# Kernel optimization log

Hardware: AMD Instinct MI355X
Metric: run time of the kernel (lower is better)

Reference implementation:

```python
import jax, jax.numpy as jnp
import numpy as np

B, S, D = 2, 2048, 2048
H, G = 32, 8            # n_head, n_kv_groups
DH = D // H             # 64
HG = H // G             # heads per group = 4


def setup_inputs() -> dict:
    key = jax.random.key(0)
    ks = jax.random.split(key, 7)
    kv_dim = G * DH
    return {
        "q": jax.random.normal(ks[0], (B, S, D), jnp.float32),
        "k": jax.random.normal(ks[1], (B, S, D), jnp.float32),
        "v": jax.random.normal(ks[2], (B, S, D), jnp.float32),
        "mask": jnp.tril(jnp.ones((S, S), jnp.bool_)),  # causal
        "w_q": jax.random.normal(ks[3], (D, D), jnp.float32) * 0.02,
        "w_k": jax.random.normal(ks[4], (kv_dim, D), jnp.float32) * 0.02,
        "w_v": jax.random.normal(ks[5], (kv_dim, D), jnp.float32) * 0.02,
        "w_out": jax.random.normal(ks[6], (D, D), jnp.float32) * 0.02,
    }


def reference(q, k, v, mask, w_q, w_k, w_v, w_out):
    scale = 1.0 / np.sqrt(DH).astype(np.float32)
    # projections (F.linear: x @ W.T)
    qp = (q @ w_q.T).reshape(B, S, G, HG, DH)   # [b s g h d]
    kp = (k @ w_k.T).reshape(B, S, G, DH)       # [b t g d]
    vp = (v @ w_v.T).reshape(B, S, G, DH)
    # grouped attention scores [b g h s t]
    scores = jnp.einsum('bsghd,btgd->bghst', qp, kp) * scale
    scores = jnp.where(mask[None, None, None], scores, jnp.float32(-jnp.inf))
    attn = jax.nn.softmax(scores, axis=-1)
    out = jnp.einsum('bghst,btgd->bsghd', attn, vp).reshape(B, S, D)
    return out @ w_out.T
```

## Files before the change

kernel.cpp:

```cpp
#include <hip/hip_runtime.h>
#include <hip/hip_bf16.h>
#include <stdint.h>

#define B_SZ 2
#define S_LEN 2048
#define D_MODEL 2048
#define NH 32
#define NG 8
#define HGRP 4
#define DHEAD 64
#define KV_DIM 512
#define M_TOK 4096
#define KVB 64
#define QBLK 256
#define N_ITEMS2 768

typedef __attribute__((ext_vector_type(8))) short bf16x8;
typedef __attribute__((ext_vector_type(4))) float f32x4;
typedef __attribute__((ext_vector_type(16))) float f32x16;

__device__ inline unsigned short f2bf(float x) {
    uint32_t u = __builtin_bit_cast(uint32_t, x);
    uint32_t r = (u + 0x7fffu + ((u >> 16) & 1u)) >> 16;
    return (unsigned short)r;
}

__device__ inline uint32_t cvtpk(float lo, float hi) {
    uint32_t r;
    asm("v_cvt_pk_bf16_f32 %0, %1, %2" : "=v"(r) : "v"(lo), "v"(hi));
    return r;
}

__device__ inline void plswap(uint32_t& a, uint32_t& b) {
    asm volatile("v_permlane32_swap_b32 %0, %1" : "+v"(a), "+v"(b));
}

__device__ inline float bf2f(unsigned short u) {
    uint32_t x = ((uint32_t)u) << 16;
    return __builtin_bit_cast(float, x);
}

__device__ inline void async_copy16(const void* g, void* l) {
    __builtin_amdgcn_global_load_lds(
        (const __attribute__((address_space(1))) void*)g,
        (__attribute__((address_space(3))) void*)l,
        16, 0, 0);
}

__device__ inline void gbar() {
    asm volatile("" ::: "memory");
    __builtin_amdgcn_s_barrier();
    asm volatile("" ::: "memory");
}
__device__ inline void lgkm0() {
    asm volatile("s_waitcnt lgkmcnt(0)" ::: "memory");
    __builtin_amdgcn_sched_barrier(0);
}

__global__ __launch_bounds__(256) void cvt_all(const float* __restrict__ q,
                                               const float* __restrict__ k,
                                               const float* __restrict__ v,
                                               const float* __restrict__ wq,
                                               const float* __restrict__ wk,
                                               const float* __restrict__ wv,
                                               const float* __restrict__ wo,
                                               unsigned short* __restrict__ qb,
                                               unsigned short* __restrict__ kb,
                                               unsigned short* __restrict__ vb,
                                               unsigned short* __restrict__ wqb,
                                               unsigned short* __restrict__ wkvb,
                                               unsigned short* __restrict__ wob,
                                               unsigned int* __restrict__ cnt) {
    const int i = blockIdx.x * 256 + threadIdx.x;
    if (i == 0) *cnt = 0u;
    const float* src; unsigned short* dst; int j;
    if (i < 1048576)      { src = q;  dst = qb;  j = i; }
    else if (i < 2097152) { src = k;  dst = kb;  j = i - 1048576; }
    else if (i < 3145728) { src = v;  dst = vb;  j = i - 2097152; }
    else if (i < 3670016) { src = wq; dst = wqb; j = i - 3145728; }
    else if (i < 3801088) { src = wk; dst = wkvb; j = i - 3670016; }
    else if (i < 3932160) { src = wv; dst = wkvb + (size_t)KV_DIM * D_MODEL; j = i - 3801088; }
    else                  { src = wo; dst = wob; j = i - 3932160; }
    const float4* p = reinterpret_cast<const float4*>(src) + (size_t)j * 2;
    float4 a = p[0], b = p[1];
    union { unsigned short u[8]; uint4 v4; } r;
    r.u[0] = f2bf(a.x); r.u[1] = f2bf(a.y); r.u[2] = f2bf(a.z); r.u[3] = f2bf(a.w);
    r.u[4] = f2bf(b.x); r.u[5] = f2bf(b.y); r.u[6] = f2bf(b.z); r.u[7] = f2bf(b.w);
    reinterpret_cast<uint4*>(dst)[j] = r.v4;
}

#define SCALE_Q 0.1803368867f
#define GK 2048

__global__ __launch_bounds__(512, 2) void gemm8p(const unsigned short* __restrict__ Aq,
                                                 const unsigned short* __restrict__ Ak,
                                                 const unsigned short* __restrict__ Av,
                                                 const unsigned short* __restrict__ Bq,
                                                 const unsigned short* __restrict__ Bkv,
                                                 unsigned short* __restrict__ out_q,
                                                 unsigned short* __restrict__ out_k,
                                                 unsigned short* __restrict__ out_v) {
    __shared__ __align__(16) char lds[131072];

    const int tid = threadIdx.x;
    const int lane = tid & 63;
    const int w = tid >> 6;
    const int wm = w >> 2, wn = w & 3;
    const int l15 = lane & 15, l4 = lane >> 4;

    int bid = blockIdx.x;
    bid = (bid & 7) * 24 + (bid >> 3);
    const int mb = bid & 15, nb = bid >> 4;
    const int m0 = mb * 256;

    const unsigned short* Ap;
    const unsigned short* Bp;
    int mode = 0, n0q = 0;
    if (nb < 8) {
        Ap = Aq; Bp = Bq + (size_t)(nb * 256) * GK; mode = 0; n0q = nb * 256;
    } else if (nb < 10) {
        Ap = Ak; Bp = Bkv + (size_t)((nb - 8) * 256) * GK; mode = 1; n0q = (nb - 8) * 256;
    } else {
        Ap = Av; Bp = Bkv + (size_t)((nb - 10) * 256 + 512) * GK; mode = 2; n0q = (nb - 10) * 256;
    }

    const int srow = tid >> 3;
    const int gcol = (((tid & 7) * 16) ^ ((srow & 7) << 4)) >> 1;
    char* const myl = lds + tid * 16;

    auto stageA = [&](int tile, int half) {
        char* dst = myl + (tile & 1) * 32768 + half * 16384;
        const unsigned short* src = Ap + (size_t)(m0 + half * 128 + srow) * GK + tile * 64 + gcol;
        async_copy16(src, dst);
        async_copy16(src + (size_t)64 * GK, dst + 8192);
    };
    auto stageB = [&](int tile, int half) {
        char* dst = myl + 65536 + (tile & 1) * 32768 + half * 16384;
        const unsigned short* src = Bp + (size_t)(half * 128 + srow) * GK + tile * 64 + gcol;
        async_copy16(src, dst);
        async_copy16(src + (size_t)64 * GK, dst + 8192);
    };

    bf16x8 af[4][2], bf[4][2];
    auto loadA = [&](int buf, int mhalf) {
        const char* base = lds + buf * 32768;
#pragma unroll
        for (int mi = 0; mi < 4; ++mi) {
            const int r = wm * 128 + mhalf * 64 + mi * 16 + l15;
#pragma unroll
            for (int ks = 0; ks < 2; ++ks)
                af[mi][ks] = *reinterpret_cast<const bf16x8*>(
                    base + r * 128 + ((ks * 64 + l4 * 16) ^ ((r & 7) << 4)));
        }
    };
    auto loadB = [&](int buf, int nhalf) {
        const char* base = lds + 65536 + buf * 32768;
#pragma unroll
        for (int ni2 = 0; ni2 < 2; ++ni2) {
            const int ni = nhalf * 2 + ni2;
            const int r = wn * 64 + ni * 16 + l15;
#pragma unroll
            for (int ks = 0; ks < 2; ++ks)
                bf[ni][ks] = *reinterpret_cast<const bf16x8*>(
                    base + r * 128 + ((ks * 64 + l4 * 16) ^ ((r & 7) << 4)));
        }
    };

    f32x4 acc[8][4] = {};
    auto mfma16 = [&](int mq, int nq) {
        __builtin_amdgcn_s_setprio(1);
#pragma unroll
        for (int mi = 0; mi < 4; ++mi)
#pragma unroll
            for (int ni2 = 0; ni2 < 2; ++ni2)
#pragma unroll
                for (int ks = 0; ks < 2; ++ks)
                    acc[mq * 4 + mi][nq * 2 + ni2] = __builtin_amdgcn_mfma_f32_16x16x32_bf16(
                        af[mi][ks], bf[nq * 2 + ni2][ks], acc[mq * 4 + mi][nq * 2 + ni2], 0, 0, 0);
        __builtin_amdgcn_s_setprio(0);
    };

    stageA(0, 0); stageA(0, 1); stageB(0, 0); stageB(0, 1); stageB(1, 0); stageB(1, 1);
    asm volatile("s_waitcnt vmcnt(4)" ::: "memory");
    gbar();

    for (int i = 0; i < 16; ++i) {
        const int u = 2 * i;
        const bool nl = (i < 15);
        loadA(0, 0); loadB(0, 0); stageA(u + 1, 0);
        gbar(); lgkm0(); mfma16(0, 0); gbar();
        loadB(0, 1); stageA(u + 1, 1);
        gbar(); lgkm0(); mfma16(0, 1); gbar();
        loadA(0, 1); if (nl) stageB(u + 2, 0);
        gbar(); lgkm0(); mfma16(1, 0); gbar();
        if (nl) stageB(u + 2, 1);
        gbar(); mfma16(1, 1);
        if (nl) asm volatile("s_waitcnt vmcnt(4)" ::: "memory");
        else    asm volatile("s_waitcnt vmcnt(0)" ::: "memory");
        gbar();
        loadA(1, 0); loadB(1, 0); if (nl) stageA(u + 2, 0);
        gbar(); lgkm0(); mfma16(0, 0); gbar();
        loadB(1, 1); if (nl) stageA(u + 2, 1);
        gbar(); lgkm0(); mfma16(0, 1); gbar();
        loadA(1, 1); if (nl) stageB(u + 3, 0);
        gbar(); lgkm0(); mfma16(1, 0); gbar();
        if (nl) stageB(u + 3, 1);
        gbar(); mfma16(1, 1);
        if (nl) asm volatile("s_waitcnt vmcnt(4)" ::: "memory");
        gbar();
    }

    if (mode == 0) {
#pragma unroll
        for (int mi = 0; mi < 8; ++mi) {
            const int row = m0 + wm * 128 + mi * 16 + l4 * 4;
#pragma unroll
            for (int ni = 0; ni < 4; ++ni) {
                const int col = n0q + wn * 64 + ni * 16 + l15;
#pragma unroll
                for (int r = 0; r < 4; ++r)
                    out_q[(size_t)(row + r) * D_MODEL + col] = f2bf(acc[mi][ni][r] * SCALE_Q);
            }
        }
    } else if (mode == 1) {
#pragma unroll
        for (int mi = 0; mi < 8; ++mi) {
            const int row = m0 + wm * 128 + mi * 16 + l4 * 4;
#pragma unroll
            for (int ni = 0; ni < 4; ++ni) {
                const int col = n0q + wn * 64 + ni * 16 + l15;
#pragma unroll
                for (int r = 0; r < 4; ++r)
                    out_k[(size_t)(row + r) * KV_DIM + col] = f2bf(acc[mi][ni][r]);
            }
        }
    } else {
        const int bb = m0 >> 11;
#pragma unroll
        for (int mi = 0; mi < 8; ++mi) {
            const int tok = (m0 & 2047) + wm * 128 + mi * 16 + l4 * 4;
#pragma unroll
            for (int ni = 0; ni < 4; ++ni) {
                const int c = n0q + wn * 64 + ni * 16 + l15;
                const int g = c >> 6, dh = c & 63;
                uint2 pk;
                pk.x = cvtpk(acc[mi][ni][0], acc[mi][ni][1]);
                pk.y = cvtpk(acc[mi][ni][2], acc[mi][ni][3]);
                *reinterpret_cast<uint2*>(out_v + (size_t)((bb * NG + g) * DHEAD + dh) * S_LEN + tok) = pk;
            }
        }
    }
}

__global__ __launch_bounds__(512, 1) void gemm8o(const unsigned short* __restrict__ A,
                                                 const unsigned short* __restrict__ B,
                                                 float* __restrict__ C) {
    __shared__ __align__(16) char lds[98304];

    const int tid = threadIdx.x;
    const int lane = tid & 63;
    const int w = tid >> 6;
    const int wm = w >> 1, wn = w & 1;
    const int l15 = lane & 15, l4 = lane >> 4;

    int bid = blockIdx.x;
    bid = (bid & 7) * 32 + (bid >> 3);
    const int mb = bid & 15, nb = bid >> 4;
    const int m0 = mb * 256, n0 = nb * 128;
    const unsigned short* Bp = B + (size_t)n0 * GK;

    const int srow = tid >> 3;
    const int gcol = (((tid & 7) * 16) ^ ((srow & 7) << 4)) >> 1;

    auto stageA = [&](int tile, int half) {
        char* dst = lds + (tile & 1) * 32768 + half * 16384 + tid * 16;
        const unsigned short* src = A + (size_t)(m0 + half * 128 + srow) * GK + tile * 64 + gcol;
        async_copy16(src, dst);
        async_copy16(src + (size_t)64 * GK, dst + 8192);
    };
    auto stageB = [&](int tile, int half) {
        char* dst = lds + 65536 + (tile & 1) * 16384 + half * 8192 + tid * 16;
        const unsigned short* src = Bp + (size_t)(half * 64 + srow) * GK + tile * 64 + gcol;
        async_copy16(src, dst);
    };

    bf16x8 af[2][2], bf[4][2];
    auto loadA2 = [&](int buf, int mhalf) {
        const char* base = lds + buf * 32768;
#pragma unroll
        for (int mi = 0; mi < 2; ++mi) {
            const int r = wm * 64 + mhalf * 32 + mi * 16 + l15;
#pragma unroll
            for (int ks = 0; ks < 2; ++ks)
                af[mi][ks] = *reinterpret_cast<const bf16x8*>(
                    base + r * 128 + ((ks * 64 + l4 * 16) ^ ((r & 7) << 4)));
        }
    };
    auto loadB2 = [&](int buf, int nhalf) {
        const char* base = lds + 65536 + buf * 16384;
#pragma unroll
        for (int ni2 = 0; ni2 < 2; ++ni2) {
            const int ni = nhalf * 2 + ni2;
            const int r = wn * 64 + ni * 16 + l15;
#pragma unroll
            for (int ks = 0; ks < 2; ++ks)
                bf[ni][ks] = *reinterpret_cast<const bf16x8*>(
                    base + r * 128 + ((ks * 64 + l4 * 16) ^ ((r & 7) << 4)));
        }
    };

    f32x4 acc[4][4] = {};
    auto mfma8 = [&](int mq, int nq) {
        __builtin_amdgcn_s_setprio(1);
#pragma unroll
        for (int mi = 0; mi < 2; ++mi)
#pragma unroll
            for (int ni2 = 0; ni2 < 2; ++ni2)
#pragma unroll
                for (int ks = 0; ks < 2; ++ks)
                    acc[mq * 2 + mi][nq * 2 + ni2] = __builtin_amdgcn_mfma_f32_16x16x32_bf16(
                        af[mi][ks], bf[nq * 2 + ni2][ks], acc[mq * 2 + mi][nq * 2 + ni2], 0, 0, 0);
        __builtin_amdgcn_s_setprio(0);
    };

    stageA(0, 0); stageA(0, 1); stageB(0, 0); stageB(0, 1); stageB(1, 0); stageB(1, 1);
    asm volatile("s_waitcnt vmcnt(2)" ::: "memory");
    gbar();

    for (int i = 0; i < 16; ++i) {
        const int u = 2 * i;
        const bool nl = (i < 15);
        loadA2(0, 0); loadB2(0, 0); stageA(u + 1, 0);
        gbar(); lgkm0(); mfma8(0, 0); gbar();
        loadB2(0, 1); stageA(u + 1, 1);
        gbar(); lgkm0(); mfma8(0, 1); gbar();
        loadA2(0, 1); if (nl) stageB(u + 2, 0);
        gbar(); lgkm0(); mfma8(1, 0); gbar();
        if (nl) stageB(u + 2, 1);
        gbar(); mfma8(1, 1);
        if (nl) asm volatile("s_waitcnt vmcnt(2)" ::: "memory");
        else    asm volatile("s_waitcnt vmcnt(0)" ::: "memory");
        gbar();
        loadA2(1, 0); loadB2(1, 0); if (nl) stageA(u + 2, 0);
        gbar(); lgkm0(); mfma8(0, 0); gbar();
        loadB2(1, 1); if (nl) stageA(u + 2, 1);
        gbar(); lgkm0(); mfma8(0, 1); gbar();
        loadA2(1, 1); if (nl) stageB(u + 3, 0);
        gbar(); lgkm0(); mfma8(1, 0); gbar();
        if (nl) stageB(u + 3, 1);
        gbar(); mfma8(1, 1);
        if (nl) asm volatile("s_waitcnt vmcnt(2)" ::: "memory");
        gbar();
    }

#pragma unroll
    for (int mi = 0; mi < 4; ++mi) {
        const int row = m0 + wm * 64 + mi * 16 + l4 * 4;
#pragma unroll
        for (int ni = 0; ni < 4; ++ni) {
            const int col = n0 + wn * 64 + ni * 16 + l15;
#pragma unroll
            for (int r = 0; r < 4; ++r)
                C[(size_t)(row + r) * D_MODEL + col] = acc[mi][ni][r];
        }
    }
}

__constant__ unsigned char cls2_qi[12]   = {7,7,3,6,6,5,5,2,4,4,1,0};
__constant__ unsigned char cls2_half[12] = {0,1,0,0,1,0,1,0,0,1,0,0};

__global__ __launch_bounds__(512, 4) void attn3_kernel(const unsigned short* __restrict__ qp,
                                                       const unsigned short* __restrict__ kp,
                                                       const unsigned short* __restrict__ vpT,
                                                       unsigned short* __restrict__ attn_out,
                                                       unsigned int* __restrict__ counter,
                                                       unsigned short* __restrict__ partO,
                                                       float* __restrict__ ml) {
    __shared__ __align__(16) unsigned short Ks[2][KVB * 64];
    __shared__ __align__(16) unsigned short Vs[2][KVB * 64];
    __shared__ int s_item;

    const int tid = threadIdx.x;
    const int lane = tid & 63;
    const int w = tid >> 6;
    const int l31 = lane & 31, hi = lane >> 5;
    const int sr = tid >> 3, sc = tid & 7;
    const int sgcol = (((sc * 16) ^ ((sr & 7) << 4)) >> 1);
    char* const kdst0 = (char*)Ks[0] + tid * 16;
    char* const kdst1 = (char*)Ks[1] + tid * 16;
    char* const vdst0 = (char*)Vs[0] + tid * 16;
    char* const vdst1 = (char*)Vs[1] + tid * 16;

    for (;;) {
        if (tid == 0) s_item = (int)atomicAdd(counter, 1u);
        __syncthreads();
        const int item = s_item;
        if (item >= N_ITEMS2) break;
        const int slot = item >> 6;
        const int bh = item & 63;
        const int qi = cls2_qi[slot];
        const int half = cls2_half[slot];
        const bool split = qi >= 4;
        const int b = bh >> 5, head = bh & 31, g = head >> 2;
        const int s0 = qi * QBLK;
        const int m = s0 + w * 32 + l31;
        const int mmaxw = s0 + w * 32 + 31;

        int j0, j1;
        if (split) { j0 = half * 2 * (qi + 1); j1 = j0 + 2 * (qi + 1); }
        else       { j0 = 0;                   j1 = 4 * (qi + 1); }

        bf16x8 qf[4];
        {
            const unsigned short* qrow = qp + (size_t)(b * S_LEN + m) * D_MODEL + head * DHEAD + hi * 8;
#pragma unroll
            for (int k = 0; k < 4; ++k)
                qf[k] = *reinterpret_cast<const bf16x8*>(qrow + k * 16);
        }

        const unsigned short* kbase = kp + (size_t)(b * S_LEN + sr) * KV_DIM + g * DHEAD + sgcol;
        const unsigned short* vbase = vpT + (size_t)((b * NG + g) * DHEAD + sr) * S_LEN + sgcol;

        float mrun = -1e30f, lrun = 0.f;
        f32x16 o0 = {}, o1 = {};

        async_copy16(kbase + (size_t)j0 * KVB * KV_DIM, kdst0);
        async_copy16(vbase + j0 * KVB, vdst0);
        asm volatile("s_waitcnt vmcnt(0)" ::: "memory");
        gbar();

        for (int j = j0; j < j1; ++j) {
            const int cur = (j - j0) & 1;
            const int t0 = j * KVB;
            if (j + 1 < j1) {
                async_copy16(kbase + (size_t)(j + 1) * KVB * KV_DIM, cur ? kdst0 : kdst1);
                async_copy16(vbase + (j + 1) * KVB, cur ? vdst0 : vdst1);
            }

            const bool tt0 = (t0 <= mmaxw);
            const bool tt1 = (t0 + 32 <= mmaxw);
            if (tt0) {
                const char* Kb = (const char*)Ks[cur];
                const char* Vb = (const char*)Vs[cur];
                const int rswz0 = (l31 & 7) << 4;

                f32x16 s0v = {}, s1v = {};
#pragma unroll
                for (int k = 0; k < 4; ++k) {
                    const int coff = k * 32 + hi * 16;
                    const bf16x8 kf0 = *reinterpret_cast<const bf16x8*>(
                        Kb + l31 * 128 + (coff ^ rswz0));
                    s0v = __builtin_amdgcn_mfma_f32_32x32x16_bf16(kf0, qf[k], s0v, 0, 0, 0);
                    if (tt1) {
                        const bf16x8 kf1 = *reinterpret_cast<const bf16x8*>(
                            Kb + (32 + l31) * 128 + (coff ^ rswz0));
                        s1v = __builtin_amdgcn_mfma_f32_32x32x16_bf16(kf1, qf[k], s1v, 0, 0, 0);
                    }
                }

                const bool msk = (t0 + KVB - 1) > (s0 + w * 32);
                float rmax = -1e30f;
                if (msk) {
#pragma unroll
                    for (int r = 0; r < 16; ++r) {
                        const int tloc = (r & 3) + 8 * (r >> 2) + 4 * hi;
                        float v = s0v[r];
                        if (t0 + tloc > m) v = -1e30f;
                        s0v[r] = v;
                        rmax = fmaxf(rmax, v);
                    }
                    if (tt1) {
#pragma unroll
                        for (int r = 0; r < 16; ++r) {
                            const int tloc = 32 + (r & 3) + 8 * (r >> 2) + 4 * hi;
                            float v = s1v[r];
                            if (t0 + tloc > m) v = -1e30f;
                            s1v[r] = v;
                            rmax = fmaxf(rmax, v);
                        }
                    }
                } else {
#pragma unroll
                    for (int r = 0; r < 16; ++r)
                        rmax = fmaxf(rmax, s0v[r]);
                    if (tt1) {
#pragma unroll
                        for (int r = 0; r < 16; ++r)
                            rmax = fmaxf(rmax, s1v[r]);
                    }
                }
                rmax = fmaxf(rmax, __shfl_xor(rmax, 32, 64));
                if (!__all(rmax <= mrun + 8.0f)) {
                    const float mnew = fmaxf(mrun, rmax);
                    const float corr = __builtin_amdgcn_exp2f(mrun - mnew);
                    lrun *= corr;
#pragma unroll
                    for (int r = 0; r < 16; ++r) { o0[r] *= corr; o1[r] *= corr; }
                    mrun = mnew;
                }
                float rs = 0.f;
#pragma unroll
                for (int r = 0; r < 16; ++r) {
                    const float p = __builtin_amdgcn_exp2f(s0v[r] - mrun);
                    s0v[r] = p;
                    rs += p;
                }
                if (tt1) {
#pragma unroll
                    for (int r = 0; r < 16; ++r) {
                        const float p = __builtin_amdgcn_exp2f(s1v[r] - mrun);
                        s1v[r] = p;
                        rs += p;
                    }
                }
                rs += __shfl_xor(rs, 32, 64);
                lrun += rs;

#pragma unroll
                for (int c = 0; c < 4; ++c) {
                    if (c >= 2 && !tt1) break;
                    const f32x16& sv = (c >> 1) ? s1v : s0v;
                    const int h8 = (c & 1) * 8;
                    uint32_t a0 = cvtpk(sv[h8 + 0], sv[h8 + 1]);
                    uint32_t a1 = cvtpk(sv[h8 + 2], sv[h8 + 3]);
                    uint32_t b0 = cvtpk(sv[h8 + 4], sv[h8 + 5]);
                    uint32_t b1 = cvtpk(sv[h8 + 6], sv[h8 + 7]);
                    plswap(a0, b0); plswap(a1, b1);
                    union { uint32_t w4[4]; bf16x8 v; } pf;
                    pf.w4[0] = a0; pf.w4[1] = a1; pf.w4[2] = b0; pf.w4[3] = b1;
                    const int coff = c * 32 + hi * 16;
                    const bf16x8 vf0 = *reinterpret_cast<const bf16x8*>(
                        Vb + l31 * 128 + (coff ^ rswz0));
                    o0 = __builtin_amdgcn_mfma_f32_32x32x16_bf16(vf0, pf.v, o0, 0, 0, 0);
                    const bf16x8 vf1 = *reinterpret_cast<const bf16x8*>(
                        Vb + (32 + l31) * 128 + (coff ^ rswz0));
                    o1 = __builtin_amdgcn_mfma_f32_32x32x16_bf16(vf1, pf.v, o1, 0, 0, 0);
                }
            }
            asm volatile("s_waitcnt vmcnt(0)" ::: "memory");
            gbar();
        }

        if (split) {
            const int pb = ((bh << 2) + (qi - 4)) * 2 + half;
            const int mrow = w * 32 + l31;
            if (hi == 0) {
                ml[pb * 512 + mrow] = mrun;
                ml[pb * 512 + 256 + mrow] = lrun;
            }
            unsigned short* dst = partO + (size_t)pb * 16384 + mrow * 64 + hi * 4;
#pragma unroll
            for (int qd = 0; qd < 4; ++qd) {
                uint2 pk0, pk1;
                pk0.x = cvtpk(o0[4 * qd + 0], o0[4 * qd + 1]);
                pk0.y = cvtpk(o0[4 * qd + 2], o0[4 * qd + 3]);
                pk1.x = cvtpk(o1[4 * qd + 0], o1[4 * qd + 1]);
                pk1.y = cvtpk(o1[4 * qd + 2], o1[4 * qd + 3]);
                *reinterpret_cast<uint2*>(dst + 8 * qd) = pk0;
                *reinterpret_cast<uint2*>(dst + 32 + 8 * qd) = pk1;
            }
        } else {
            const float inv = 1.0f / lrun;
            unsigned short* dst = attn_out + (size_t)(b * S_LEN + m) * D_MODEL + head * DHEAD + hi * 4;
#pragma unroll
            for (int qd = 0; qd < 4; ++qd) {
                uint2 pk0, pk1;
                pk0.x = cvtpk(o0[4 * qd + 0] * inv, o0[4 * qd + 1] * inv);
                pk0.y = cvtpk(o0[4 * qd + 2] * inv, o0[4 * qd + 3] * inv);
                pk1.x = cvtpk(o1[4 * qd + 0] * inv, o1[4 * qd + 1] * inv);
                pk1.y = cvtpk(o1[4 * qd + 2] * inv, o1[4 * qd + 3] * inv);
                *reinterpret_cast<uint2*>(dst + 8 * qd) = pk0;
                *reinterpret_cast<uint2*>(dst + 32 + 8 * qd) = pk1;
            }
        }
    }
}

__global__ __launch_bounds__(512) void merge2_kernel(const unsigned short* __restrict__ partO,
                                                     const float* __restrict__ ml,
                                                     unsigned short* __restrict__ attn_out) {
    const int blk = blockIdx.x;
    const int bh = blk >> 2;
    const int qi = (blk & 3) + 4;
    const int b = bh >> 5, head = bh & 31;
    const int s0 = qi * QBLK;
    const int tid = threadIdx.x;
    const int row = tid >> 1, dh0 = (tid & 1) * 32;
    const int pb0 = blk * 2, pb1 = pb0 + 1;

    const float m0 = ml[pb0 * 512 + row], l0 = ml[pb0 * 512 + 256 + row];
    const float m1 = ml[pb1 * 512 + row], l1 = ml[pb1 * 512 + 256 + row];
    const float M = fmaxf(m0, m1);
    float w0 = __builtin_amdgcn_exp2f(m0 - M);
    float w1 = __builtin_amdgcn_exp2f(m1 - M);
    const float inv = 1.0f / (l0 * w0 + l1 * w1);
    w0 *= inv; w1 *= inv;

    const uint4* p0 = reinterpret_cast<const uint4*>(partO + (size_t)pb0 * 16384 + row * 64 + dh0);
    const uint4* p1 = reinterpret_cast<const uint4*>(partO + (size_t)pb1 * 16384 + row * 64 + dh0);
    unsigned short* dst = attn_out + (size_t)(b * S_LEN + s0 + row) * D_MODEL + head * DHEAD + dh0;
#pragma unroll
    for (int c = 0; c < 4; ++c) {
        union { unsigned short u[8]; uint4 v; } ua, ub, uo;
        ua.v = p0[c]; ub.v = p1[c];
#pragma unroll
        for (int e = 0; e < 8; e += 2) {
            float x0 = bf2f(ua.u[e]) * w0 + bf2f(ub.u[e]) * w1;
            float x1 = bf2f(ua.u[e + 1]) * w0 + bf2f(ub.u[e + 1]) * w1;
            reinterpret_cast<uint32_t*>(uo.u)[e >> 1] = cvtpk(x0, x1);
        }
        reinterpret_cast<uint4*>(dst)[c] = uo.v;
    }
}

extern "C" void kernel_launch(void* const* d_in, const int* in_sizes, int n_in,
                              void* d_out, int out_size, void* d_ws, size_t ws_size,
                              hipStream_t stream) {
    const float* q     = (const float*)d_in[0];
    const float* k     = (const float*)d_in[1];
    const float* v     = (const float*)d_in[2];
    const float* w_q   = (const float*)d_in[4];
    const float* w_k   = (const float*)d_in[5];
    const float* w_v   = (const float*)d_in[6];
    const float* w_out = (const float*)d_in[7];

    char* ws = (char*)d_ws;
    size_t off = 0;
    auto alloc = [&](size_t n) { char* p = ws + off; off += (n + 255) & ~(size_t)255; return p; };
    unsigned short* qb   = (unsigned short*)alloc((size_t)M_TOK * D_MODEL * 2);
    unsigned short* kb   = (unsigned short*)alloc((size_t)M_TOK * D_MODEL * 2);
    unsigned short* vb   = (unsigned short*)alloc((size_t)M_TOK * D_MODEL * 2);
    unsigned short* wqb  = (unsigned short*)alloc((size_t)D_MODEL * D_MODEL * 2);
    unsigned short* wkvb = (unsigned short*)alloc((size_t)2 * KV_DIM * D_MODEL * 2);
    unsigned short* wob  = (unsigned short*)alloc((size_t)D_MODEL * D_MODEL * 2);
    unsigned short* qpb  = (unsigned short*)alloc((size_t)M_TOK * D_MODEL * 2);
    unsigned short* kpb  = (unsigned short*)alloc((size_t)M_TOK * KV_DIM * 2);
    unsigned short* vtb  = (unsigned short*)alloc((size_t)M_TOK * KV_DIM * 2);
    unsigned short* aob  = (unsigned short*)alloc((size_t)M_TOK * D_MODEL * 2);
    float*          mlb  = (float*)alloc((size_t)512 * 512 * 4);
    unsigned int*   cnt  = (unsigned int*)alloc(256);

    cvt_all<<<dim3(17408), dim3(256), 0, stream>>>(q, k, v, w_q, w_k, w_v, w_out,
                                                   qb, kb, vb, wqb, wkvb, wob, cnt);

    gemm8p<<<dim3(192), dim3(512), 0, stream>>>(qb, kb, vb, wqb, wkvb, qpb, kpb, vtb);

    attn3_kernel<<<dim3(768), dim3(512), 0, stream>>>(qpb, kpb, vtb, aob, cnt, qb, mlb);
    merge2_kernel<<<dim3(256), dim3(512), 0, stream>>>(qb, mlb, aob);

    gemm8o<<<dim3(256), dim3(512), 0, stream>>>(aob, wob, (float*)d_out);
}
```

Before: 189.3 us.

## Double attention KV block to 128 keys per iteration, halve persistent grid

The attention kernel now loads 128 keys per iteration instead of 64, storing V with 256-byte rows and computing four 32-key score tiles per step. This halves the number of barriers and loop iterations per work item and gives each sync more MFMA work. In exchange it doubles LDS use and register pressure (launch bounds lowered to 2 blocks/CU, grid reduced to 512). It also makes causal-boundary waste coarser, since a 128-key block can be partly masked.

```diff
diff --git a/kernel.cpp b/kernel.cpp
--- a/kernel.cpp
+++ b/kernel.cpp
@@ -11,7 +11,7 @@
 #define DHEAD 64
 #define KV_DIM 512
 #define M_TOK 4096
-#define KVB 64
+#define KVB2 128
 #define QBLK 256
 #define N_ITEMS2 768
 
@@ -369,23 +369,26 @@
 __constant__ unsigned char cls2_qi[12]   = {7,7,3,6,6,5,5,2,4,4,1,0};
 __constant__ unsigned char cls2_half[12] = {0,1,0,0,1,0,1,0,0,1,0,0};
 
-__global__ __launch_bounds__(512, 4) void attn3_kernel(const unsigned short* __restrict__ qp,
+__global__ __launch_bounds__(512, 2) void attn4_kernel(const unsigned short* __restrict__ qp,
                                                        const unsigned short* __restrict__ kp,
                                                        const unsigned short* __restrict__ vpT,
                                                        unsigned short* __restrict__ attn_out,
                                                        unsigned int* __restrict__ counter,
                                                        unsigned short* __restrict__ partO,
                                                        float* __restrict__ ml) {
-    __shared__ __align__(16) unsigned short Ks[2][KVB * 64];
-    __shared__ __align__(16) unsigned short Vs[2][KVB * 64];
+    __shared__ __align__(16) unsigned short Ks[2][KVB2 * 64];
+    __shared__ __align__(16) unsigned short Vs[2][64 * KVB2];
     __shared__ int s_item;
 
     const int tid = threadIdx.x;
     const int lane = tid & 63;
     const int w = tid >> 6;
     const int l31 = lane & 31, hi = lane >> 5;
-    const int sr = tid >> 3, sc = tid & 7;
-    const int sgcol = (((sc * 16) ^ ((sr & 7) << 4)) >> 1);
+
+    const int ksr = tid >> 3, ksc = tid & 7;
+    const int vsr = tid >> 4, vsc = tid & 15;
+    const int kgcol = (((ksc * 16) ^ ((ksr & 7) << 4)) >> 1);
+    const int vgcol = (((vsc * 16) ^ ((vsr & 7) << 4)) >> 1);
     char* const kdst0 = (char*)Ks[0] + tid * 16;
     char* const kdst1 = (char*)Ks[1] + tid * 16;
     char* const vdst0 = (char*)Vs[0] + tid * 16;
@@ -404,11 +407,12 @@
         const int b = bh >> 5, head = bh & 31, g = head >> 2;
         const int s0 = qi * QBLK;
         const int m = s0 + w * 32 + l31;
-        const int mmaxw = s0 + w * 32 + 31;
+        const int mmin = s0 + w * 32;
+        const int mmaxw = mmin + 31;
 
         int j0, j1;
-        if (split) { j0 = half * 2 * (qi + 1); j1 = j0 + 2 * (qi + 1); }
-        else       { j0 = 0;                   j1 = 4 * (qi + 1); }
+        if (split) { j0 = half * (qi + 1); j1 = j0 + (qi + 1); }
+        else       { j0 = 0;               j1 = 2 * (qi + 1); }
 
         bf16x8 qf[4];
         {
@@ -418,75 +422,73 @@
                 qf[k] = *reinterpret_cast<const bf16x8*>(qrow + k * 16);
         }
 
-        const unsigned short* kbase = kp + (size_t)(b * S_LEN + sr) * KV_DIM + g * DHEAD + sgcol;
-        const unsigned short* vbase = vpT + (size_t)((b * NG + g) * DHEAD + sr) * S_LEN + sgcol;
+        const unsigned short* kbase = kp + (size_t)(b * S_LEN + ksr) * KV_DIM + g * DHEAD + kgcol;
+        const unsigned short* vbase = vpT + (size_t)((b * NG + g) * DHEAD + vsr) * S_LEN + vgcol;
 
         float mrun = -1e30f, lrun = 0.f;
         f32x16 o0 = {}, o1 = {};
 
-        async_copy16(kbase + (size_t)j0 * KVB * KV_DIM, kdst0);
-        async_copy16(vbase + j0 * KVB, vdst0);
+        async_copy16(kbase + (size_t)j0 * KVB2 * KV_DIM, kdst0);
+        async_copy16(kbase + (size_t)(j0 * KVB2 + 64) * KV_DIM, kdst0 + 8192);
+        async_copy16(vbase + j0 * KVB2, vdst0);
+        async_copy16(vbase + (size_t)32 * S_LEN + j0 * KVB2, vdst0 + 8192);
         asm volatile("s_waitcnt vmcnt(0)" ::: "memory");
         gbar();
 
         for (int j = j0; j < j1; ++j) {
             const int cur = (j - j0) & 1;
-            const int t0 = j * KVB;
+            const int t0 = j * KVB2;
             if (j + 1 < j1) {
-                async_copy16(kbase + (size_t)(j + 1) * KVB * KV_DIM, cur ? kdst0 : kdst1);
-                async_copy16(vbase + (j + 1) * KVB, cur ? vdst0 : vdst1);
-            }
-
-            const bool tt0 = (t0 <= mmaxw);
-            const bool tt1 = (t0 + 32 <= mmaxw);
-            if (tt0) {
+                char* kd = cur ? kdst0 : kdst1;
+                char* vd = cur ? vdst0 : vdst1;
+                async_copy16(kbase + (size_t)(j + 1) * KVB2 * KV_DIM, kd);
+                async_copy16(kbase + (size_t)((j + 1) * KVB2 + 64) * KV_DIM, kd + 8192);
+                async_copy16(vbase + (j + 1) * KVB2, vd);
+                async_copy16(vbase + (size_t)32 * S_LEN + (j + 1) * KVB2, vd + 8192);
+            }
+
+            if (t0 <= mmaxw) {
                 const char* Kb = (const char*)Ks[cur];
                 const char* Vb = (const char*)Vs[cur];
-                const int rswz0 = (l31 & 7) << 4;
-
-                f32x16 s0v = {}, s1v = {};
+                const int rswz = (l31 & 7) << 4;
+
+                bool cmp[4], emk[4];
+#pragma unroll
+                for (int tt = 0; tt < 4; ++tt) {
+                    cmp[tt] = (t0 + 32 * tt) <= mmaxw;
+                    emk[tt] = (t0 + 32 * tt + 31) > mmin;
+                }
+
+                f32x16 sv[4] = {};
 #pragma unroll
                 for (int k = 0; k < 4; ++k) {
                     const int coff = k * 32 + hi * 16;
-                    const bf16x8 kf0 = *reinterpret_cast<const bf16x8*>(
-                        Kb + l31 * 128 + (coff ^ rswz0));
-                    s0v = __builtin_amdgcn_mfma_f32_32x32x16_bf16(kf0, qf[k], s0v, 0, 0, 0);
-                    if (tt1) {
-                        const bf16x8 kf1 = *reinterpret_cast<const bf16x8*>(
-                            Kb + (32 + l31) * 128 + (coff ^ rswz0));
-                        s1v = __builtin_amdgcn_mfma_f32_32x32x16_bf16(kf1, qf[k], s1v, 0, 0, 0);
+#pragma unroll
+                    for (int tt = 0; tt < 4; ++tt) {
+                        if (!cmp[tt]) continue;
+                        const bf16x8 kf = *reinterpret_cast<const bf16x8*>(
+                            Kb + (tt * 32 + l31) * 128 + (coff ^ rswz));
+                        sv[tt] = __builtin_amdgcn_mfma_f32_32x32x16_bf16(kf, qf[k], sv[tt], 0, 0, 0);
                     }
                 }
 
-                const bool msk = (t0 + KVB - 1) > (s0 + w * 32);
                 float rmax = -1e30f;
-                if (msk) {
-#pragma unroll
-                    for (int r = 0; r < 16; ++r) {
-                        const int tloc = (r & 3) + 8 * (r >> 2) + 4 * hi;
-                        float v = s0v[r];
-                        if (t0 + tloc > m) v = -1e30f;
-                        s0v[r] = v;
-                        rmax = fmaxf(rmax, v);
-                    }
-                    if (tt1) {
+#pragma unroll
+                for (int tt = 0; tt < 4; ++tt) {
+                    if (!cmp[tt]) continue;
+                    if (emk[tt]) {
 #pragma unroll
                         for (int r = 0; r < 16; ++r) {
-                            const int tloc = 32 + (r & 3) + 8 * (r >> 2) + 4 * hi;
-                            float v = s1v[r];
+                            const int tloc = tt * 32 + (r & 3) + 8 * (r >> 2) + 4 * hi;
+                            float v = sv[tt][r];
                             if (t0 + tloc > m) v = -1e30f;
-                            s1v[r] = v;
+                            sv[tt][r] = v;
                             rmax = fmaxf(rmax, v);
                         }
-                    }
-                } else {
-#pragma unroll
-                    for (int r = 0; r < 16; ++r)
-                        rmax = fmaxf(rmax, s0v[r]);
-                    if (tt1) {
+                    } else {
 #pragma unroll
                         for (int r = 0; r < 16; ++r)
-                            rmax = fmaxf(rmax, s1v[r]);
+                            rmax = fmaxf(rmax, sv[tt][r]);
                     }
                 }
                 rmax = fmaxf(rmax, __shfl_xor(rmax, 32, 64));
@@ -500,16 +502,12 @@
                 }
                 float rs = 0.f;
 #pragma unroll
-                for (int r = 0; r < 16; ++r) {
-                    const float p = __builtin_amdgcn_exp2f(s0v[r] - mrun);
-                    s0v[r] = p;
-                    rs += p;
-                }
-                if (tt1) {
+                for (int tt = 0; tt < 4; ++tt) {
+                    if (!cmp[tt]) continue;
 #pragma unroll
                     for (int r = 0; r < 16; ++r) {
-                        const float p = __builtin_amdgcn_exp2f(s1v[r] - mrun);
-                        s1v[r] = p;
+                        const float p = __builtin_amdgcn_exp2f(sv[tt][r] - mrun);
+                        sv[tt][r] = p;
                         rs += p;
                     }
                 }
@@ -517,23 +515,23 @@
                 lrun += rs;
 
 #pragma unroll
-                for (int c = 0; c < 4; ++c) {
-                    if (c >= 2 && !tt1) break;
-                    const f32x16& sv = (c >> 1) ? s1v : s0v;
+                for (int c = 0; c < 8; ++c) {
+                    const int tt = c >> 1;
+                    if (!cmp[tt]) continue;
                     const int h8 = (c & 1) * 8;
-                    uint32_t a0 = cvtpk(sv[h8 + 0], sv[h8 + 1]);
-                    uint32_t a1 = cvtpk(sv[h8 + 2], sv[h8 + 3]);
-                    uint32_t b0 = cvtpk(sv[h8 + 4], sv[h8 + 5]);
-                    uint32_t b1 = cvtpk(sv[h8 + 6], sv[h8 + 7]);
+                    uint32_t a0 = cvtpk(sv[tt][h8 + 0], sv[tt][h8 + 1]);
+                    uint32_t a1 = cvtpk(sv[tt][h8 + 2], sv[tt][h8 + 3]);
+                    uint32_t b0 = cvtpk(sv[tt][h8 + 4], sv[tt][h8 + 5]);
+                    uint32_t b1 = cvtpk(sv[tt][h8 + 6], sv[tt][h8 + 7]);
                     plswap(a0, b0); plswap(a1, b1);
                     union { uint32_t w4[4]; bf16x8 v; } pf;
                     pf.w4[0] = a0; pf.w4[1] = a1; pf.w4[2] = b0; pf.w4[3] = b1;
                     const int coff = c * 32 + hi * 16;
                     const bf16x8 vf0 = *reinterpret_cast<const bf16x8*>(
-                        Vb + l31 * 128 + (coff ^ rswz0));
+                        Vb + l31 * 256 + (coff ^ rswz));
                     o0 = __builtin_amdgcn_mfma_f32_32x32x16_bf16(vf0, pf.v, o0, 0, 0, 0);
                     const bf16x8 vf1 = *reinterpret_cast<const bf16x8*>(
-                        Vb + (32 + l31) * 128 + (coff ^ rswz0));
+                        Vb + (32 + l31) * 256 + (coff ^ rswz));
                     o1 = __builtin_amdgcn_mfma_f32_32x32x16_bf16(vf1, pf.v, o1, 0, 0, 0);
                 }
             }
@@ -645,7 +643,7 @@
 
     gemm8p<<<dim3(192), dim3(512), 0, stream>>>(qb, kb, vb, wqb, wkvb, qpb, kpb, vtb);
 
-    attn3_kernel<<<dim3(768), dim3(512), 0, stream>>>(qpb, kpb, vtb, aob, cnt, qb, mlb);
+    attn4_kernel<<<dim3(512), dim3(512), 0, stream>>>(qpb, kpb, vtb, aob, cnt, qb, mlb);
     merge2_kernel<<<dim3(256), dim3(512), 0, stream>>>(qb, mlb, aob);
 
     gemm8o<<<dim3(256), dim3(512), 0, stream>>>(aob, wob, (float*)d_out);
```

Result: slower. 201.2 us (+6.3%).

## Replace atomic work queue with static split-KV schedule and three-way merge

Applied to the files above, without the earlier changes.

The attention kernel no longer pulls work items from an atomic counter. It now launches one block per item over a fixed 16-slot table that splits longer query blocks (qi≥2) into 2 or 3 KV chunks of roughly equal length. The merge kernel combines 2 or 3 partial results per query block, and the partial/ml buffers now reuse the bf16 k and q workspaces, so the counter reset is dropped. The goal is better load balance and no atomic or loop overhead, at the cost of more partial outputs to write and merge.

```diff
diff --git a/kernel.cpp b/kernel.cpp
--- a/kernel.cpp
+++ b/kernel.cpp
@@ -13,7 +13,6 @@
 #define M_TOK 4096
 #define KVB 64
 #define QBLK 256
-#define N_ITEMS2 768
 
 typedef __attribute__((ext_vector_type(8))) short bf16x8;
 typedef __attribute__((ext_vector_type(4))) float f32x4;
@@ -69,10 +68,8 @@
                                                unsigned short* __restrict__ vb,
                                                unsigned short* __restrict__ wqb,
                                                unsigned short* __restrict__ wkvb,
-                                               unsigned short* __restrict__ wob,
-                                               unsigned int* __restrict__ cnt) {
+                                               unsigned short* __restrict__ wob) {
     const int i = blockIdx.x * 256 + threadIdx.x;
-    if (i == 0) *cnt = 0u;
     const float* src; unsigned short* dst; int j;
     if (i < 1048576)      { src = q;  dst = qb;  j = i; }
     else if (i < 2097152) { src = k;  dst = kb;  j = i - 1048576; }
@@ -366,19 +363,19 @@
     }
 }
 
-__constant__ unsigned char cls2_qi[12]   = {7,7,3,6,6,5,5,2,4,4,1,0};
-__constant__ unsigned char cls2_half[12] = {0,1,0,0,1,0,1,0,0,1,0,0};
-
-__global__ __launch_bounds__(512, 4) void attn3_kernel(const unsigned short* __restrict__ qp,
+__constant__ unsigned char sl_qi[16] = {7,7,7,6,6,6,5,5,4,4,3,3,2,2,1,0};
+__constant__ unsigned char sl_j0[16] = {0,11,22,0,10,19,0,11,0,10,0,8,0,6,0,0};
+__constant__ unsigned char sl_j1[16] = {11,22,32,10,19,28,11,24,10,20,8,16,6,12,8,4};
+__constant__ unsigned char sl_pt[16] = {0,1,2,0,1,2,0,1,0,1,0,1,0,1,0,0};
+
+__global__ __launch_bounds__(512, 4) void attn5_kernel(const unsigned short* __restrict__ qp,
                                                        const unsigned short* __restrict__ kp,
                                                        const unsigned short* __restrict__ vpT,
                                                        unsigned short* __restrict__ attn_out,
-                                                       unsigned int* __restrict__ counter,
                                                        unsigned short* __restrict__ partO,
                                                        float* __restrict__ ml) {
     __shared__ __align__(16) unsigned short Ks[2][KVB * 64];
     __shared__ __align__(16) unsigned short Vs[2][KVB * 64];
-    __shared__ int s_item;
 
     const int tid = threadIdx.x;
     const int lane = tid & 63;
@@ -391,222 +388,228 @@
     char* const vdst0 = (char*)Vs[0] + tid * 16;
     char* const vdst1 = (char*)Vs[1] + tid * 16;
 
-    for (;;) {
-        if (tid == 0) s_item = (int)atomicAdd(counter, 1u);
-        __syncthreads();
-        const int item = s_item;
-        if (item >= N_ITEMS2) break;
-        const int slot = item >> 6;
-        const int bh = item & 63;
-        const int qi = cls2_qi[slot];
-        const int half = cls2_half[slot];
-        const bool split = qi >= 4;
-        const int b = bh >> 5, head = bh & 31, g = head >> 2;
-        const int s0 = qi * QBLK;
-        const int m = s0 + w * 32 + l31;
-        const int mmaxw = s0 + w * 32 + 31;
-
-        int j0, j1;
-        if (split) { j0 = half * 2 * (qi + 1); j1 = j0 + 2 * (qi + 1); }
-        else       { j0 = 0;                   j1 = 4 * (qi + 1); }
-
-        bf16x8 qf[4];
-        {
-            const unsigned short* qrow = qp + (size_t)(b * S_LEN + m) * D_MODEL + head * DHEAD + hi * 8;
-#pragma unroll
-            for (int k = 0; k < 4; ++k)
-                qf[k] = *reinterpret_cast<const bf16x8*>(qrow + k * 16);
-        }
-
-        const unsigned short* kbase = kp + (size_t)(b * S_LEN + sr) * KV_DIM + g * DHEAD + sgcol;
-        const unsigned short* vbase = vpT + (size_t)((b * NG + g) * DHEAD + sr) * S_LEN + sgcol;
-
-        float mrun = -1e30f, lrun = 0.f;
-        f32x16 o0 = {}, o1 = {};
-
-        async_copy16(kbase + (size_t)j0 * KVB * KV_DIM, kdst0);
-        async_copy16(vbase + j0 * KVB, vdst0);
+    const int item = blockIdx.x;
+    const int slot = item >> 6;
+    const int bh = item & 63;
+    const int qi = sl_qi[slot];
+    const int j0 = sl_j0[slot];
+    const int j1 = sl_j1[slot];
+    const int part = sl_pt[slot];
+    const bool merged = (qi >= 2);
+    const int b = bh >> 5, head = bh & 31, g = head >> 2;
+    const int s0 = qi * QBLK;
+    const int m = s0 + w * 32 + l31;
+    const int mmin = s0 + w * 32;
+    const int mmaxw = mmin + 31;
+
+    bf16x8 qf[4];
+    {
+        const unsigned short* qrow = qp + (size_t)(b * S_LEN + m) * D_MODEL + head * DHEAD + hi * 8;
+#pragma unroll
+        for (int k = 0; k < 4; ++k)
+            qf[k] = *reinterpret_cast<const bf16x8*>(qrow + k * 16);
+    }
+
+    const unsigned short* kbase = kp + (size_t)(b * S_LEN + sr) * KV_DIM + g * DHEAD + sgcol;
+    const unsigned short* vbase = vpT + (size_t)((b * NG + g) * DHEAD + sr) * S_LEN + sgcol;
+
+    float mrun = -1e30f, lrun = 0.f;
+    f32x16 o0 = {}, o1 = {};
+
+    async_copy16(kbase + (size_t)j0 * KVB * KV_DIM, kdst0);
+    async_copy16(vbase + j0 * KVB, vdst0);
+    asm volatile("s_waitcnt vmcnt(0)" ::: "memory");
+    gbar();
+
+    for (int j = j0; j < j1; ++j) {
+        const int cur = (j - j0) & 1;
+        const int t0 = j * KVB;
+        if (j + 1 < j1) {
+            async_copy16(kbase + (size_t)(j + 1) * KVB * KV_DIM, cur ? kdst0 : kdst1);
+            async_copy16(vbase + (j + 1) * KVB, cur ? vdst0 : vdst1);
+        }
+
+        const bool tt0 = (t0 <= mmaxw);
+        const bool tt1 = (t0 + 32 <= mmaxw);
+        if (tt0) {
+            const char* Kb = (const char*)Ks[cur];
+            const char* Vb = (const char*)Vs[cur];
+            const int rswz0 = (l31 & 7) << 4;
+
+            f32x16 s0v = {}, s1v = {};
+#pragma unroll
+            for (int k = 0; k < 4; ++k) {
+                const int coff = k * 32 + hi * 16;
+                const bf16x8 kf0 = *reinterpret_cast<const bf16x8*>(
+                    Kb + l31 * 128 + (coff ^ rswz0));
+                s0v = __builtin_amdgcn_mfma_f32_32x32x16_bf16(kf0, qf[k], s0v, 0, 0, 0);
+                if (tt1) {
+                    const bf16x8 kf1 = *reinterpret_cast<const bf16x8*>(
+                        Kb + (32 + l31) * 128 + (coff ^ rswz0));
+                    s1v = __builtin_amdgcn_mfma_f32_32x32x16_bf16(kf1, qf[k], s1v, 0, 0, 0);
+                }
+            }
+
+            const bool msk = (t0 + KVB - 1) > mmin;
+            float rmax = -1e30f;
+            if (msk) {
+#pragma unroll
+                for (int r = 0; r < 16; ++r) {
+                    const int tloc = (r & 3) + 8 * (r >> 2) + 4 * hi;
+                    float v = s0v[r];
+                    if (t0 + tloc > m) v = -1e30f;
+                    s0v[r] = v;
+                    rmax = fmaxf(rmax, v);
+                }
+                if (tt1) {
+#pragma unroll
+                    for (int r = 0; r < 16; ++r) {
+                        const int tloc = 32 + (r & 3) + 8 * (r >> 2) + 4 * hi;
+                        float v = s1v[r];
+                        if (t0 + tloc > m) v = -1e30f;
+                        s1v[r] = v;
+                        rmax = fmaxf(rmax, v);
+                    }
+                }
+            } else {
+#pragma unroll
+                for (int r = 0; r < 16; ++r)
+                    rmax = fmaxf(rmax, s0v[r]);
+                if (tt1) {
+#pragma unroll
+                    for (int r = 0; r < 16; ++r)
+                        rmax = fmaxf(rmax, s1v[r]);
+                }
+            }
+            rmax = fmaxf(rmax, __shfl_xor(rmax, 32, 64));
+            if (!__all(rmax <= mrun + 8.0f)) {
+                const float mnew = fmaxf(mrun, rmax);
+                const float corr = __builtin_amdgcn_exp2f(mrun - mnew);
+                lrun *= corr;
+#pragma unroll
+                for (int r = 0; r < 16; ++r) { o0[r] *= corr; o1[r] *= corr; }
+                mrun = mnew;
+            }
+            float rs = 0.f;
+#pragma unroll
+            for (int r = 0; r < 16; ++r) {
+                const float p = __builtin_amdgcn_exp2f(s0v[r] - mrun);
+                s0v[r] = p;
+                rs += p;
+            }
+            if (tt1) {
+#pragma unroll
+                for (int r = 0; r < 16; ++r) {
+                    const float p = __builtin_amdgcn_exp2f(s1v[r] - mrun);
+                    s1v[r] = p;
+                    rs += p;
+                }
+            }
+            rs += __shfl_xor(rs, 32, 64);
+            lrun += rs;
+
+#pragma unroll
+            for (int c = 0; c < 4; ++c) {
+                if (c >= 2 && !tt1) break;
+                const f32x16& sv = (c >> 1) ? s1v : s0v;
+                const int h8 = (c & 1) * 8;
+                uint32_t a0 = cvtpk(sv[h8 + 0], sv[h8 + 1]);
+                uint32_t a1 = cvtpk(sv[h8 + 2], sv[h8 + 3]);
+                uint32_t b0 = cvtpk(sv[h8 + 4], sv[h8 + 5]);
+                uint32_t b1 = cvtpk(sv[h8 + 6], sv[h8 + 7]);
+                plswap(a0, b0); plswap(a1, b1);
+                union { uint32_t w4[4]; bf16x8 v; } pf;
+                pf.w4[0] = a0; pf.w4[1] = a1; pf.w4[2] = b0; pf.w4[3] = b1;
+                const int coff = c * 32 + hi * 16;
+                const bf16x8 vf0 = *reinterpret_cast<const bf16x8*>(
+                    Vb + l31 * 128 + (coff ^ rswz0));
+                o0 = __builtin_amdgcn_mfma_f32_32x32x16_bf16(vf0, pf.v, o0, 0, 0, 0);
+                const bf16x8 vf1 = *reinterpret_cast<const bf16x8*>(
+                    Vb + (32 + l31) * 128 + (coff ^ rswz0));
+                o1 = __builtin_amdgcn_mfma_f32_32x32x16_bf16(vf1, pf.v, o1, 0, 0, 0);
+            }
+        }
         asm volatile("s_waitcnt vmcnt(0)" ::: "memory");
         gbar();
-
-        for (int j = j0; j < j1; ++j) {
-            const int cur = (j - j0) & 1;
-            const int t0 = j * KVB;
-            if (j + 1 < j1) {
-                async_copy16(kbase + (size_t)(j + 1) * KVB * KV_DIM, cur ? kdst0 : kdst1);
-                async_copy16(vbase + (j + 1) * KVB, cur ? vdst0 : vdst1);
-            }
-
-            const bool tt0 = (t0 <= mmaxw);
-            const bool tt1 = (t0 + 32 <= mmaxw);
-            if (tt0) {
-                const char* Kb = (const char*)Ks[cur];
-                const char* Vb = (const char*)Vs[cur];
-                const int rswz0 = (l31 & 7) << 4;
-
-                f32x16 s0v = {}, s1v = {};
-#pragma unroll
-                for (int k = 0; k < 4; ++k) {
-                    const int coff = k * 32 + hi * 16;
-                    const bf16x8 kf0 = *reinterpret_cast<const bf16x8*>(
-                        Kb + l31 * 128 + (coff ^ rswz0));
-                    s0v = __builtin_amdgcn_mfma_f32_32x32x16_bf16(kf0, qf[k], s0v, 0, 0, 0);
-                    if (tt1) {
-                        const bf16x8 kf1 = *reinterpret_cast<const bf16x8*>(
-                            Kb + (32 + l31) * 128 + (coff ^ rswz0));
-                        s1v = __builtin_amdgcn_mfma_f32_32x32x16_bf16(kf1, qf[k], s1v, 0, 0, 0);
-                    }
-                }
-
-                const bool msk = (t0 + KVB - 1) > (s0 + w * 32);
-                float rmax = -1e30f;
-                if (msk) {
-#pragma unroll
-                    for (int r = 0; r < 16; ++r) {
-                        const int tloc = (r & 3) + 8 * (r >> 2) + 4 * hi;
-                        float v = s0v[r];
-                        if (t0 + tloc > m) v = -1e30f;
-                        s0v[r] = v;
-                        rmax = fmaxf(rmax, v);
-                    }
-                    if (tt1) {
-#pragma unroll
-                        for (int r = 0; r < 16; ++r) {
-                            const int tloc = 32 + (r & 3) + 8 * (r >> 2) + 4 * hi;
-                            float v = s1v[r];
-                            if (t0 + tloc > m) v = -1e30f;
-                            s1v[r] = v;
-                            rmax = fmaxf(rmax, v);
-                        }
-                    }
-                } else {
-#pragma unroll
-                    for (int r = 0; r < 16; ++r)
-                        rmax = fmaxf(rmax, s0v[r]);
-                    if (tt1) {
-#pragma unroll
-                        for (int r = 0; r < 16; ++r)
-                            rmax = fmaxf(rmax, s1v[r]);
-                    }
-                }
-                rmax = fmaxf(rmax, __shfl_xor(rmax, 32, 64));
-                if (!__all(rmax <= mrun + 8.0f)) {
-                    const float mnew = fmaxf(mrun, rmax);
-                    const float corr = __builtin_amdgcn_exp2f(mrun - mnew);
-                    lrun *= corr;
-#pragma unroll
-                    for (int r = 0; r < 16; ++r) { o0[r] *= corr; o1[r] *= corr; }
-                    mrun = mnew;
-                }
-                float rs = 0.f;
-#pragma unroll
-                for (int r = 0; r < 16; ++r) {
-                    const float p = __builtin_amdgcn_exp2f(s0v[r] - mrun);
-                    s0v[r] = p;
-                    rs += p;
-                }
-                if (tt1) {
-#pragma unroll
-                    for (int r = 0; r < 16; ++r) {
-                        const float p = __builtin_amdgcn_exp2f(s1v[r] - mrun);
-                        s1v[r] = p;
-                        rs += p;
-                    }
-                }
-                rs += __shfl_xor(rs, 32, 64);
-                lrun += rs;
-
-#pragma unroll
-                for (int c = 0; c < 4; ++c) {
-                    if (c >= 2 && !tt1) break;
-                    const f32x16& sv = (c >> 1) ? s1v : s0v;
-                    const int h8 = (c & 1) * 8;
-                    uint32_t a0 = cvtpk(sv[h8 + 0], sv[h8 + 1]);
-                    uint32_t a1 = cvtpk(sv[h8 + 2], sv[h8 + 3]);
-                    uint32_t b0 = cvtpk(sv[h8 + 4], sv[h8 + 5]);
-                    uint32_t b1 = cvtpk(sv[h8 + 6], sv[h8 + 7]);
-                    plswap(a0, b0); plswap(a1, b1);
-                    union { uint32_t w4[4]; bf16x8 v; } pf;
-                    pf.w4[0] = a0; pf.w4[1] = a1; pf.w4[2] = b0; pf.w4[3] = b1;
-                    const int coff = c * 32 + hi * 16;
-                    const bf16x8 vf0 = *reinterpret_cast<const bf16x8*>(
-                        Vb + l31 * 128 + (coff ^ rswz0));
-                    o0 = __builtin_amdgcn_mfma_f32_32x32x16_bf16(vf0, pf.v, o0, 0, 0, 0);
-                    const bf16x8 vf1 = *reinterpret_cast<const bf16x8*>(
-                        Vb + (32 + l31) * 128 + (coff ^ rswz0));
-                    o1 = __builtin_amdgcn_mfma_f32_32x32x16_bf16(vf1, pf.v, o1, 0, 0, 0);
-                }
-            }
-            asm volatile("s_waitcnt vmcnt(0)" ::: "memory");
-            gbar();
-        }
-
-        if (split) {
-            const int pb = ((bh << 2) + (qi - 4)) * 2 + half;
-            const int mrow = w * 32 + l31;
-            if (hi == 0) {
-                ml[pb * 512 + mrow] = mrun;
-                ml[pb * 512 + 256 + mrow] = lrun;
-            }
-            unsigned short* dst = partO + (size_t)pb * 16384 + mrow * 64 + hi * 4;
-#pragma unroll
-            for (int qd = 0; qd < 4; ++qd) {
-                uint2 pk0, pk1;
-                pk0.x = cvtpk(o0[4 * qd + 0], o0[4 * qd + 1]);
-                pk0.y = cvtpk(o0[4 * qd + 2], o0[4 * qd + 3]);
-                pk1.x = cvtpk(o1[4 * qd + 0], o1[4 * qd + 1]);
-                pk1.y = cvtpk(o1[4 * qd + 2], o1[4 * qd + 3]);
-                *reinterpret_cast<uint2*>(dst + 8 * qd) = pk0;
-                *reinterpret_cast<uint2*>(dst + 32 + 8 * qd) = pk1;
-            }
-        } else {
-            const float inv = 1.0f / lrun;
-            unsigned short* dst = attn_out + (size_t)(b * S_LEN + m) * D_MODEL + head * DHEAD + hi * 4;
-#pragma unroll
-            for (int qd = 0; qd < 4; ++qd) {
-                uint2 pk0, pk1;
-                pk0.x = cvtpk(o0[4 * qd + 0] * inv, o0[4 * qd + 1] * inv);
-                pk0.y = cvtpk(o0[4 * qd + 2] * inv, o0[4 * qd + 3] * inv);
-                pk1.x = cvtpk(o1[4 * qd + 0] * inv, o1[4 * qd + 1] * inv);
-                pk1.y = cvtpk(o1[4 * qd + 2] * inv, o1[4 * qd + 3] * inv);
-                *reinterpret_cast<uint2*>(dst + 8 * qd) = pk0;
-                *reinterpret_cast<uint2*>(dst + 32 + 8 * qd) = pk1;
-            }
-        }
-    }
-}
-
-__global__ __launch_bounds__(512) void merge2_kernel(const unsigned short* __restrict__ partO,
+    }
+
+    if (merged) {
+        const int base = 2 * (qi - 2) + (qi == 7 ? 1 : 0);
+        const int pb = bh * 14 + base + part;
+        const int mrow = w * 32 + l31;
+        if (hi == 0) {
+            ml[pb * 512 + mrow] = mrun;
+            ml[pb * 512 + 256 + mrow] = lrun;
+        }
+        unsigned short* dst = partO + (size_t)pb * 16384 + mrow * 64 + hi * 4;
+#pragma unroll
+        for (int qd = 0; qd < 4; ++qd) {
+            uint2 pk0, pk1;
+            pk0.x = cvtpk(o0[4 * qd + 0], o0[4 * qd + 1]);
+            pk0.y = cvtpk(o0[4 * qd + 2], o0[4 * qd + 3]);
+            pk1.x = cvtpk(o1[4 * qd + 0], o1[4 * qd + 1]);
+            pk1.y = cvtpk(o1[4 * qd + 2], o1[4 * qd + 3]);
+            *reinterpret_cast<uint2*>(dst + 8 * qd) = pk0;
+            *reinterpret_cast<uint2*>(dst + 32 + 8 * qd) = pk1;
+        }
+    } else {
+        const float inv = 1.0f / lrun;
+        unsigned short* dst = attn_out + (size_t)(b * S_LEN + m) * D_MODEL + head * DHEAD + hi * 4;
+#pragma unroll
+        for (int qd = 0; qd < 4; ++qd) {
+            uint2 pk0, pk1;
+            pk0.x = cvtpk(o0[4 * qd + 0] * inv, o0[4 * qd + 1] * inv);
+            pk0.y = cvtpk(o0[4 * qd + 2] * inv, o0[4 * qd + 3] * inv);
+            pk1.x = cvtpk(o1[4 * qd + 0] * inv, o1[4 * qd + 1] * inv);
+            pk1.y = cvtpk(o1[4 * qd + 2] * inv, o1[4 * qd + 3] * inv);
+            *reinterpret_cast<uint2*>(dst + 8 * qd) = pk0;
+            *reinterpret_cast<uint2*>(dst + 32 + 8 * qd) = pk1;
+        }
+    }
+}
+
+__global__ __launch_bounds__(512) void merge3_kernel(const unsigned short* __restrict__ partO,
                                                      const float* __restrict__ ml,
                                                      unsigned short* __restrict__ attn_out) {
     const int blk = blockIdx.x;
-    const int bh = blk >> 2;
-    const int qi = (blk & 3) + 4;
+    const int bh = blk / 6;
+    const int qi = 2 + (blk - bh * 6);
+    const int np = (qi >= 6) ? 3 : 2;
+    const int base = 2 * (qi - 2) + (qi == 7 ? 1 : 0);
+    const int pb = bh * 14 + base;
     const int b = bh >> 5, head = bh & 31;
     const int s0 = qi * QBLK;
     const int tid = threadIdx.x;
     const int row = tid >> 1, dh0 = (tid & 1) * 32;
-    const int pb0 = blk * 2, pb1 = pb0 + 1;
-
-    const float m0 = ml[pb0 * 512 + row], l0 = ml[pb0 * 512 + 256 + row];
-    const float m1 = ml[pb1 * 512 + row], l1 = ml[pb1 * 512 + 256 + row];
-    const float M = fmaxf(m0, m1);
+
+    float m0 = ml[(pb + 0) * 512 + row], l0 = ml[(pb + 0) * 512 + 256 + row];
+    float m1 = ml[(pb + 1) * 512 + row], l1 = ml[(pb + 1) * 512 + 256 + row];
+    float m2 = -1e30f, l2 = 0.f;
+    if (np == 3) { m2 = ml[(pb + 2) * 512 + row]; l2 = ml[(pb + 2) * 512 + 256 + row]; }
+    const float M = fmaxf(fmaxf(m0, m1), m2);
     float w0 = __builtin_amdgcn_exp2f(m0 - M);
     float w1 = __builtin_amdgcn_exp2f(m1 - M);
-    const float inv = 1.0f / (l0 * w0 + l1 * w1);
-    w0 *= inv; w1 *= inv;
-
-    const uint4* p0 = reinterpret_cast<const uint4*>(partO + (size_t)pb0 * 16384 + row * 64 + dh0);
-    const uint4* p1 = reinterpret_cast<const uint4*>(partO + (size_t)pb1 * 16384 + row * 64 + dh0);
+    float w2 = (np == 3) ? __builtin_amdgcn_exp2f(m2 - M) : 0.f;
+    const float inv = 1.0f / (l0 * w0 + l1 * w1 + l2 * w2);
+    w0 *= inv; w1 *= inv; w2 *= inv;
+
+    const uint4* p0 = reinterpret_cast<const uint4*>(partO + (size_t)(pb + 0) * 16384 + row * 64 + dh0);
+    const uint4* p1 = reinterpret_cast<const uint4*>(partO + (size_t)(pb + 1) * 16384 + row * 64 + dh0);
+    const uint4* p2 = reinterpret_cast<const uint4*>(partO + (size_t)(pb + 2) * 16384 + row * 64 + dh0);
     unsigned short* dst = attn_out + (size_t)(b * S_LEN + s0 + row) * D_MODEL + head * DHEAD + dh0;
 #pragma unroll
     for (int c = 0; c < 4; ++c) {
-        union { unsigned short u[8]; uint4 v; } ua, ub, uo;
+        union { unsigned short u[8]; uint4 v; } ua, ub, uc, uo;
         ua.v = p0[c]; ub.v = p1[c];
+        if (np == 3) uc.v = p2[c];
 #pragma unroll
         for (int e = 0; e < 8; e += 2) {
             float x0 = bf2f(ua.u[e]) * w0 + bf2f(ub.u[e]) * w1;
             float x1 = bf2f(ua.u[e + 1]) * w0 + bf2f(ub.u[e + 1]) * w1;
+            if (np == 3) {
+                x0 += bf2f(uc.u[e]) * w2;
+                x1 += bf2f(uc.u[e + 1]) * w2;
+            }
             reinterpret_cast<uint32_t*>(uo.u)[e >> 1] = cvtpk(x0, x1);
         }
         reinterpret_cast<uint4*>(dst)[c] = uo.v;
@@ -637,16 +640,14 @@
     unsigned short* kpb  = (unsigned short*)alloc((size_t)M_TOK * KV_DIM * 2);
     unsigned short* vtb  = (unsigned short*)alloc((size_t)M_TOK * KV_DIM * 2);
     unsigned short* aob  = (unsigned short*)alloc((size_t)M_TOK * D_MODEL * 2);
-    float*          mlb  = (float*)alloc((size_t)512 * 512 * 4);
-    unsigned int*   cnt  = (unsigned int*)alloc(256);
 
     cvt_all<<<dim3(17408), dim3(256), 0, stream>>>(q, k, v, w_q, w_k, w_v, w_out,
-                                                   qb, kb, vb, wqb, wkvb, wob, cnt);
+                                                   qb, kb, vb, wqb, wkvb, wob);
 
     gemm8p<<<dim3(192), dim3(512), 0, stream>>>(qb, kb, vb, wqb, wkvb, qpb, kpb, vtb);
 
-    attn3_kernel<<<dim3(768), dim3(512), 0, stream>>>(qpb, kpb, vtb, aob, cnt, qb, mlb);
-    merge2_kernel<<<dim3(256), dim3(512), 0, stream>>>(qb, mlb, aob);
+    attn5_kernel<<<dim3(1024), dim3(512), 0, stream>>>(qpb, kpb, vtb, aob, kb, (float*)qb);
+    merge3_kernel<<<dim3(384), dim3(512), 0, stream>>>(kb, (float*)qb, aob);
 
     gemm8o<<<dim3(256), dim3(512), 0, stream>>>(aob, wob, (float*)d_out);
 }
```

After: 190.9 us (median of 2 runs). Within noise of the previous version (+0.9%).
